# Kernel optimization log

Measured on AMD Instinct MI355X. Metric: run time of the kernel, lower is better.

Reference implementation:

```python
import jax, jax.numpy as jnp
import numpy as np

N_NODES = 100_000
N_EDGES = 6_400_000
THETA = 1.0          # firing threshold
W_SCALE = 0.1        # synaptic weight scale


def setup_inputs() -> dict:
    key = jax.random.key(0)
    k1, k2, k3, k4 = jax.random.split(key, 4)
    src = jax.random.randint(k1, (N_EDGES,), 0, N_NODES)
    dst = jax.random.randint(k2, (N_EDGES,), 0, N_NODES)
    edge_index = jnp.stack([src, dst]).astype(jnp.int64)  # [2, E]
    W = jax.random.normal(k3, (N_EDGES,), dtype=jnp.float32) * W_SCALE
    x = jax.random.uniform(k4, (N_NODES, 1), dtype=jnp.float32)  # initial state window
    return {"x": x, "W": W, "edge_index": edge_index,
            "n_steps": 200, "equilibration_steps": 100}


def _layer(x, src, dst, W):
    # x: [n_nodes, hist]; current spike state is last column (as in x[:, -1])
    s = x[:, -1]
    # synaptic input: scatter-add of weighted presynaptic activity over edges
    inp = jax.ops.segment_sum(W * s[src], dst, num_segments=N_NODES)
    s_new = jax.nn.sigmoid(inp - THETA)  # surrogate spike nonlinearity
    # roll the history window
    return jnp.concatenate([x[:, 1:], s_new[:, None]], axis=1)


def reference(x, W, edge_index, n_steps, equilibration_steps):
    src, dst = edge_index[0], edge_index[1]

    def step(carry, _):
        nxt = _layer(carry, src, dst, W)
        return nxt, nxt[:, -1]

    # equilibration phase (outputs discarded, mirrors _equilibrate)
    x, _ = jax.lax.scan(step, x, None, length=equilibration_steps)
    # recorded simulation phase; dense spike raster replaces the dynamic
    # nonzero()+cat spike log (same information, jit-compatible shape)
    _, raster = jax.lax.scan(step, x, None, length=n_steps)
    return raster  # [n_steps, n_nodes]
```

## Files before the change

### kernel.cpp

```cpp
#include <hip/hip_runtime.h>
#include <math.h>

#define N_NODES 100000
#define N_EDGES 6400000
#define THETA 1.0f
#define EQ_STEPS 100
#define N_STEPS 200
#define TOTAL_STEPS (EQ_STEPS + N_STEPS)

#define NG 1563
#define NRANK (NG * 64)
#define NBINS 512
#define SPLIT 51200
#define C0BYTES 51200
#define C1BYTES 49152
#define S8_BYTES 100352
#define SELL_CAP 10000000
#define WQ_SCALE (32767.0f / 0.75f)
#define QSCALE   (0.75f / (32767.0f * 255.0f))


__global__ __launch_bounds__(256) void deg_kernel(const int* __restrict__ dst,
                                                  int* __restrict__ deg) {
    int stride = gridDim.x * blockDim.x;
    for (int e = blockIdx.x * blockDim.x + threadIdx.x; e < N_EDGES; e += stride)
        atomicAdd(&deg[dst[e]], 1);
}

__global__ __launch_bounds__(256) void binhist_kernel(const int* __restrict__ deg,
                                                      int* __restrict__ bins) {
    int n = blockIdx.x * blockDim.x + threadIdx.x;
    if (n < N_NODES) {
        int d = deg[n]; if (d > NBINS - 1) d = NBINS - 1;
        atomicAdd(&bins[d], 1);
    }
}

__global__ __launch_bounds__(NBINS) void binscan_kernel(const int* __restrict__ bins,
                                                        int* __restrict__ bincur) {
    __shared__ int s[NBINS];
    int t = threadIdx.x;
    s[t] = bins[t];
    __syncthreads();
    for (int o = 1; o < NBINS; o <<= 1) {
        int v = (t >= o) ? s[t - o] : 0;
        __syncthreads();
        s[t] += v;
        __syncthreads();
    }
    bincur[t] = (t == 0) ? 0 : s[t - 1];
}

__global__ __launch_bounds__(256) void perm_kernel(const int* __restrict__ deg,
                                                   int* __restrict__ bincur,
                                                   int* __restrict__ perm,
                                                   int* __restrict__ rank) {
    int n = blockIdx.x * blockDim.x + threadIdx.x;
    if (n < N_NODES) {
        int d = deg[n]; if (d > NBINS - 1) d = NBINS - 1;
        int pos = atomicAdd(&bincur[d], 1);
        perm[pos] = n;
        rank[n] = pos;
    }
}

__global__ __launch_bounds__(256) void degf_kernel(const int* __restrict__ src,
                                                   const int* __restrict__ dst,
                                                   const int* __restrict__ rank,
                                                   int* __restrict__ degf) {
    int stride = gridDim.x * blockDim.x;
    for (int e = blockIdx.x * blockDim.x + threadIdx.x; e < N_EDGES; e += stride) {
        int f = (rank[src[e]] >= SPLIT) ? 1 : 0;
        atomicAdd(&degf[(dst[e] << 1) | f], 1);
    }
}

__global__ __launch_bounds__(256) void width_kernel(const int* __restrict__ degf,
                                                    const int* __restrict__ perm,
                                                    int* __restrict__ gw0,
                                                    int* __restrict__ gw1) {
    int g = blockIdx.x * blockDim.x + threadIdx.x;
    if (g >= NG) return;
    int m0 = 0, m1 = 0;
    for (int j = 0; j < 64; ++j) {
        int r = (g << 6) + j;
        if (r < N_NODES) {
            int n = perm[r];
            int d0 = degf[n << 1], d1 = degf[(n << 1) | 1];
            if (d0 > m0) m0 = d0;
            if (d1 > m1) m1 = d1;
        }
    }
    gw0[g] = (m0 + 3) & ~3;
    gw1[g] = (m1 + 3) & ~3;
}

__global__ __launch_bounds__(1024) void colptr_kernel(const int* __restrict__ gw0,
                                                      const int* __restrict__ gw1,
                                                      int* __restrict__ colptr) {
    __shared__ int sums[1024];
    const int T = 1024;
    int t = threadIdx.x;
    const int PER = (NG + T - 1) / T;
    int b = t * PER;
    int e = b + PER; if (e > NG) e = NG;
    int s = 0;
    for (int i = b; i < e; ++i) s += gw0[i] + gw1[i];
    sums[t] = s;
    __syncthreads();
    for (int o = 1; o < T; o <<= 1) {
        int v = (t >= o) ? sums[t - o] : 0;
        __syncthreads();
        sums[t] += v;
        __syncthreads();
    }
    int base = (t == 0) ? 0 : sums[t - 1];
    for (int i = b; i < e; ++i) {
        colptr[i] = base << 6;
        base += gw0[i] + gw1[i];
    }
    if (t == T - 1) colptr[NG] = base << 6;
}


__global__ __launch_bounds__(256) void sell_scatter_kernel(
        const int* __restrict__ src, const int* __restrict__ dst,
        const float* __restrict__ W,
        const int* __restrict__ rank, const int* __restrict__ colptr,
        const int* __restrict__ gw0,
        int* __restrict__ cnt2, int* __restrict__ sell) {
    int stride = gridDim.x * blockDim.x;
    for (int e = blockIdx.x * blockDim.x + threadIdx.x; e < N_EDGES; e += stride) {
        int d = dst[e];
        int rs = rank[src[e]];
        int f = (rs >= SPLIT) ? 1 : 0;
        int sl = rs - f * SPLIT;
        int k = atomicAdd(&cnt2[(d << 1) | f], 1);
        int rd = rank[d];
        int g = rd >> 6;
        float w = W[e] * WQ_SCALE;
        w = fminf(fmaxf(w, -32767.f), 32767.f);
        int wq = __float2int_rn(w);
        int slot = colptr[g] + ((f ? gw0[g] : 0) << 6)
                 + ((k >> 2) << 8) + ((rd & 63) << 2) + (k & 3);
        sell[slot] = (wq << 16) | sl;
    }
}

__global__ __launch_bounds__(256) void pad_kernel(const int* __restrict__ degf,
                                                  const int* __restrict__ perm,
                                                  const int* __restrict__ colptr,
                                                  const int* __restrict__ gw0,
                                                  int* __restrict__ sell) {
    int r = (blockIdx.x * blockDim.x + threadIdx.x) >> 6;
    int lane = threadIdx.x & 63;
    if (r >= NRANK) return;
    int g = r >> 6;
    int base = colptr[g];
    int w0 = gw0[g];
    int w1 = ((colptr[g + 1] - base) >> 6) - w0;
    int d0 = 0, d1 = 0;
    if (r < N_NODES) {
        int n = perm[r];
        d0 = degf[n << 1]; d1 = degf[(n << 1) | 1];
    }
    int c = (r & 63) << 2;
    for (int k = d0 + lane; k < w0; k += 64)
        sell[base + ((k >> 2) << 8) + c + (k & 3)] = 0;
    int base1 = base + (w0 << 6);
    for (int k = d1 + lane; k < w1; k += 64)
        sell[base1 + ((k >> 2) << 8) + c + (k & 3)] = 0;
}

__global__ __launch_bounds__(256) void initq_kernel(const float* __restrict__ x,
                                                    const int* __restrict__ rank,
                                                    unsigned char* __restrict__ s8) {
    int n = blockIdx.x * blockDim.x + threadIdx.x;
    if (n < N_NODES) {
        float v = fminf(fmaxf(x[n], 0.f), 1.f);
        s8[rank[n]] = (unsigned char)__float2int_rn(v * 255.0f);
    }
}

__global__ __launch_bounds__(1024, 8) void step_kernel(
        const int* __restrict__ sell, const int* __restrict__ colptr,
        const int* __restrict__ gw0, const int* __restrict__ perm,
        const unsigned char* __restrict__ s8_in,
        unsigned char* __restrict__ s8_out,
        float* __restrict__ out_row) {
    __shared__ int4 sc4[C0BYTES / 16];
    __shared__ float red[4][4][64];
    const unsigned char* sc = (const unsigned char*)sc4;
    int tid = threadIdx.x;
    int wv = tid >> 6, lane = tid & 63;
    int gsub = wv >> 2;
    int q = wv & 3;
    int gid = NG - 1 - ((blockIdx.x << 2) + gsub);
    bool active = (gid >= 0);
    int base = 0, wid0 = 0, wid1 = 0;
    if (active) {
        int c0 = colptr[gid], c1 = colptr[gid + 1];
        wid0 = gw0[gid];
        wid1 = ((c1 - c0) >> 6) - wid0;
        base = c0;
    }
    float a0 = 0.f, a1 = 0.f, a2 = 0.f, a3 = 0.f;

    {
        const int4* gp = (const int4*)s8_in;
        for (int i = tid; i < C0BYTES / 16; i += 1024) sc4[i] = gp[i];
    }
    __syncthreads();
    if (active) {
        const int4* col = (const int4*)(sell + base) + lane;
        int n4 = wid0 >> 2;
        #pragma unroll 2
        for (int k = q; k < n4; k += 4) {
            int4 p = col[k << 6];
            a0 = fmaf((float)__mul24(p.x >> 16, (int)sc[p.x & 0xFFFF]), QSCALE, a0);
            a1 = fmaf((float)__mul24(p.y >> 16, (int)sc[p.y & 0xFFFF]), QSCALE, a1);
            a2 = fmaf((float)__mul24(p.z >> 16, (int)sc[p.z & 0xFFFF]), QSCALE, a2);
            a3 = fmaf((float)__mul24(p.w >> 16, (int)sc[p.w & 0xFFFF]), QSCALE, a3);
        }
    }
    __syncthreads();

    {
        const int4* gp = (const int4*)(s8_in + C0BYTES);
        for (int i = tid; i < C1BYTES / 16; i += 1024) sc4[i] = gp[i];
    }
    __syncthreads();
    if (active) {
        const int4* col = (const int4*)(sell + base + (wid0 << 6)) + lane;
        int n4 = wid1 >> 2;
        #pragma unroll 2
        for (int k = q; k < n4; k += 4) {
            int4 p = col[k << 6];
            a0 = fmaf((float)__mul24(p.x >> 16, (int)sc[p.x & 0xFFFF]), QSCALE, a0);
            a1 = fmaf((float)__mul24(p.y >> 16, (int)sc[p.y & 0xFFFF]), QSCALE, a1);
            a2 = fmaf((float)__mul24(p.z >> 16, (int)sc[p.z & 0xFFFF]), QSCALE, a2);
            a3 = fmaf((float)__mul24(p.w >> 16, (int)sc[p.w & 0xFFFF]), QSCALE, a3);
        }
    }
    float acc = (a0 + a1) + (a2 + a3);
    if (q != 0) red[gsub][q][lane] = acc;
    __syncthreads();
    if (q == 0 && active) {
        acc += red[gsub][1][lane] + red[gsub][2][lane] + red[gsub][3][lane];
        int r = (gid << 6) + lane;
        if (r < N_NODES) {
            float v = 1.0f / (1.0f + __expf(-(acc - THETA)));
            s8_out[r] = (unsigned char)__float2int_rn(v * 255.0f);
            if (out_row) out_row[perm[r]] = v;
        }
    }
}

extern "C" void kernel_launch(void* const* d_in, const int* in_sizes, int n_in,
                              void* d_out, int out_size, void* d_ws, size_t ws_size,
                              hipStream_t stream) {
    const float* x  = (const float*)d_in[0];
    const float* W  = (const float*)d_in[1];
    const int*   ei = (const int*)d_in[2];
    const int*   src = ei;
    const int*   dst = ei + N_EDGES;

    char* w = (char*)d_ws;
    size_t o = 0;
    auto alloc = [&](size_t bytes) { char* p = w + o; o = (o + bytes + 511) & ~(size_t)511; return p; };
    int* deg    = (int*)alloc(N_NODES * sizeof(int));
    int* degf   = (int*)alloc((size_t)N_NODES * 2 * sizeof(int));
    int* bins   = (int*)alloc(NBINS * sizeof(int));
    int* bincur = (int*)alloc(NBINS * sizeof(int));
    int* perm   = (int*)alloc(NRANK * sizeof(int));
    int* rank   = (int*)alloc(N_NODES * sizeof(int));
    int* gw0    = (int*)alloc(NG * sizeof(int));
    int* gw1    = (int*)alloc(NG * sizeof(int));
    int* colptr = (int*)alloc((NG + 1) * sizeof(int));
    int* cnt2   = (int*)alloc((size_t)N_NODES * 2 * sizeof(int));
    int* sell   = (int*)alloc((size_t)SELL_CAP * sizeof(int));
    unsigned char* s8a = (unsigned char*)alloc(S8_BYTES);
    unsigned char* s8b = (unsigned char*)alloc(S8_BYTES);

    hipMemsetAsync(deg,  0, N_NODES * sizeof(int), stream);
    hipMemsetAsync(degf, 0, (size_t)N_NODES * 2 * sizeof(int), stream);
    hipMemsetAsync(bins, 0, NBINS * sizeof(int), stream);
    hipMemsetAsync(cnt2, 0, (size_t)N_NODES * 2 * sizeof(int), stream);

    const int NB256 = (N_NODES + 255) / 256;
    deg_kernel<<<1024, 256, 0, stream>>>(dst, deg);
    binhist_kernel<<<NB256, 256, 0, stream>>>(deg, bins);
    binscan_kernel<<<1, NBINS, 0, stream>>>(bins, bincur);
    perm_kernel<<<NB256, 256, 0, stream>>>(deg, bincur, perm, rank);
    degf_kernel<<<1024, 256, 0, stream>>>(src, dst, rank, degf);
    width_kernel<<<(NG + 255) / 256, 256, 0, stream>>>(degf, perm, gw0, gw1);
    colptr_kernel<<<1, 1024, 0, stream>>>(gw0, gw1, colptr);
    sell_scatter_kernel<<<2048, 256, 0, stream>>>(src, dst, W, rank, colptr, gw0, cnt2, sell);
    pad_kernel<<<(NRANK * 64 + 255) / 256, 256, 0, stream>>>(degf, perm, colptr, gw0, sell);
    initq_kernel<<<NB256, 256, 0, stream>>>(x, rank, s8a);

    float* outBase = (float*)d_out;
    unsigned char* bufs[2] = {s8a, s8b};
    const int SGRID = (NG + 3) / 4;
    for (int t = 0; t < TOTAL_STEPS; ++t) {
        unsigned char* cur = bufs[t & 1];
        unsigned char* nxt = bufs[(t + 1) & 1];
        float* outrow = (t >= EQ_STEPS) ? (outBase + (size_t)(t - EQ_STEPS) * N_NODES)
                                        : nullptr;
        step_kernel<<<SGRID, 1024, 0, stream>>>(sell, colptr, gw0, perm, cur, nxt, outrow);
    }
}
```

Baseline: 3.901 ms.

## Balance step-kernel work across blocks and waves by nonzero count

Adds a setup kernel that binary-searches the column pointer so each of 512 blocks gets a contiguous range of row groups holding roughly equal numbers of packed entries. Inside the step kernel, each of the 16 waves takes an even slice of the block's 4-wide work units. Partial sums are combined per group with shared-memory atomics. The aim is to remove load imbalance between blocks and waves. In exchange, each step launches more blocks, so the 100 KB state is staged into shared memory more times in total, and segment tracking plus LDS atomics add overhead. Any block whose range covers more than 16 groups would silently drop the extra groups.

New measurement: 5.587 ms. 1.43x slower.

```diff
diff --git a/kernel.cpp b/kernel.cpp
--- a/kernel.cpp
+++ b/kernel.cpp
@@ -16,6 +16,8 @@
 #define C1BYTES 49152
 #define S8_BYTES 100352
 #define SELL_CAP 10000000
+#define NSB 512
+#define NGPB 16
 #define WQ_SCALE (32767.0f / 0.75f)
 #define QSCALE   (0.75f / (32767.0f * 255.0f))
 
@@ -120,6 +122,20 @@
         base += gw0[i] + gw1[i];
     }
     if (t == T - 1) colptr[NG] = base << 6;
+}
+
+__global__ __launch_bounds__(NSB) void blockmap_kernel(const int* __restrict__ colptr,
+                                                       int* __restrict__ bstart) {
+    long long TS = colptr[NG];
+    int b = threadIdx.x;
+    int lo = 0, hi = NG;
+    while (lo < hi) {
+        int mid = (lo + hi) >> 1;
+        if ((long long)colptr[mid] * NSB < (long long)b * TS) lo = mid + 1;
+        else hi = mid;
+    }
+    bstart[b] = lo;
+    if (b == 0) bstart[NSB] = NG;
 }
 
 
@@ -185,42 +201,70 @@
 __global__ __launch_bounds__(1024, 8) void step_kernel(
         const int* __restrict__ sell, const int* __restrict__ colptr,
         const int* __restrict__ gw0, const int* __restrict__ perm,
+        const int* __restrict__ bstart,
         const unsigned char* __restrict__ s8_in,
         unsigned char* __restrict__ s8_out,
         float* __restrict__ out_row) {
     __shared__ int4 sc4[C0BYTES / 16];
-    __shared__ float red[4][4][64];
+    __shared__ float red[NGPB][64];
+    __shared__ int sb0[NGPB], sb1[NGPB], sn0[NGPB], sn1[NGPB];
+    __shared__ int sq0[NGPB + 1], sq1[NGPB + 1];
     const unsigned char* sc = (const unsigned char*)sc4;
     int tid = threadIdx.x;
     int wv = tid >> 6, lane = tid & 63;
-    int gsub = wv >> 2;
-    int q = wv & 3;
-    int gid = NG - 1 - ((blockIdx.x << 2) + gsub);
-    bool active = (gid >= 0);
-    int base = 0, wid0 = 0, wid1 = 0;
-    if (active) {
-        int c0 = colptr[gid], c1 = colptr[gid + 1];
-        wid0 = gw0[gid];
-        wid1 = ((c1 - c0) >> 6) - wid0;
-        base = c0;
-    }
-    float a0 = 0.f, a1 = 0.f, a2 = 0.f, a3 = 0.f;
+
+    int glo = bstart[blockIdx.x];
+    int ghi = bstart[blockIdx.x + 1];
+    int ng = ghi - glo; if (ng > NGPB) ng = NGPB;
 
     {
         const int4* gp = (const int4*)s8_in;
         for (int i = tid; i < C0BYTES / 16; i += 1024) sc4[i] = gp[i];
     }
-    __syncthreads();
-    if (active) {
-        const int4* col = (const int4*)(sell + base) + lane;
-        int n4 = wid0 >> 2;
-        #pragma unroll 2
-        for (int k = q; k < n4; k += 4) {
-            int4 p = col[k << 6];
-            a0 = fmaf((float)__mul24(p.x >> 16, (int)sc[p.x & 0xFFFF]), QSCALE, a0);
-            a1 = fmaf((float)__mul24(p.y >> 16, (int)sc[p.y & 0xFFFF]), QSCALE, a1);
-            a2 = fmaf((float)__mul24(p.z >> 16, (int)sc[p.z & 0xFFFF]), QSCALE, a2);
-            a3 = fmaf((float)__mul24(p.w >> 16, (int)sc[p.w & 0xFFFF]), QSCALE, a3);
+    if (tid < NGPB * 64) ((float*)red)[tid] = 0.f;
+    if (tid < ng) {
+        int g = glo + tid;
+        int c0 = colptr[g], c1 = colptr[g + 1];
+        int w0 = gw0[g];
+        sb0[tid] = c0;
+        sb1[tid] = c0 + (w0 << 6);
+        sn0[tid] = w0 >> 2;
+        sn1[tid] = (((c1 - c0) >> 6) - w0) >> 2;
+    }
+    __syncthreads();
+    if (tid == 0) {
+        int q0 = 0, q1 = 0;
+        for (int i = 0; i < ng; ++i) {
+            sq0[i] = q0; q0 += sn0[i];
+            sq1[i] = q1; q1 += sn1[i];
+        }
+        sq0[ng] = q0; sq1[ng] = q1;
+    }
+    __syncthreads();
+
+    {
+        int U = sq0[ng];
+        int lo = (wv * U) >> 4, hi = ((wv + 1) * U) >> 4;
+        if (lo < hi) {
+            int seg = 0;
+            while (lo >= sq0[seg + 1]) ++seg;
+            float a0 = 0.f, a1 = 0.f, a2 = 0.f, a3 = 0.f;
+            for (int u = lo; u < hi; ++u) {
+                if (u >= sq0[seg + 1]) {
+                    atomicAdd(&red[seg][lane], (a0 + a1) + (a2 + a3));
+                    a0 = a1 = a2 = a3 = 0.f;
+                    ++seg;
+                    while (u >= sq0[seg + 1]) ++seg;
+                }
+                const int4* cp = (const int4*)(sell + sb0[seg])
+                               + ((u - sq0[seg]) << 6) + lane;
+                int4 pk = *cp;
+                a0 = fmaf((float)__mul24(pk.x >> 16, (int)sc[pk.x & 0xFFFF]), QSCALE, a0);
+                a1 = fmaf((float)__mul24(pk.y >> 16, (int)sc[pk.y & 0xFFFF]), QSCALE, a1);
+                a2 = fmaf((float)__mul24(pk.z >> 16, (int)sc[pk.z & 0xFFFF]), QSCALE, a2);
+                a3 = fmaf((float)__mul24(pk.w >> 16, (int)sc[pk.w & 0xFFFF]), QSCALE, a3);
+            }
+            atomicAdd(&red[seg][lane], (a0 + a1) + (a2 + a3));
         }
     }
     __syncthreads();
@@ -230,26 +274,37 @@
         for (int i = tid; i < C1BYTES / 16; i += 1024) sc4[i] = gp[i];
     }
     __syncthreads();
-    if (active) {
-        const int4* col = (const int4*)(sell + base + (wid0 << 6)) + lane;
-        int n4 = wid1 >> 2;
-        #pragma unroll 2
-        for (int k = q; k < n4; k += 4) {
-            int4 p = col[k << 6];
-            a0 = fmaf((float)__mul24(p.x >> 16, (int)sc[p.x & 0xFFFF]), QSCALE, a0);
-            a1 = fmaf((float)__mul24(p.y >> 16, (int)sc[p.y & 0xFFFF]), QSCALE, a1);
-            a2 = fmaf((float)__mul24(p.z >> 16, (int)sc[p.z & 0xFFFF]), QSCALE, a2);
-            a3 = fmaf((float)__mul24(p.w >> 16, (int)sc[p.w & 0xFFFF]), QSCALE, a3);
-        }
-    }
-    float acc = (a0 + a1) + (a2 + a3);
-    if (q != 0) red[gsub][q][lane] = acc;
-    __syncthreads();
-    if (q == 0 && active) {
-        acc += red[gsub][1][lane] + red[gsub][2][lane] + red[gsub][3][lane];
-        int r = (gid << 6) + lane;
+    {
+        int U = sq1[ng];
+        int lo = (wv * U) >> 4, hi = ((wv + 1) * U) >> 4;
+        if (lo < hi) {
+            int seg = 0;
+            while (lo >= sq1[seg + 1]) ++seg;
+            float a0 = 0.f, a1 = 0.f, a2 = 0.f, a3 = 0.f;
+            for (int u = lo; u < hi; ++u) {
+                if (u >= sq1[seg + 1]) {
+                    atomicAdd(&red[seg][lane], (a0 + a1) + (a2 + a3));
+                    a0 = a1 = a2 = a3 = 0.f;
+                    ++seg;
+                    while (u >= sq1[seg + 1]) ++seg;
+                }
+                const int4* cp = (const int4*)(sell + sb1[seg])
+                               + ((u - sq1[seg]) << 6) + lane;
+                int4 pk = *cp;
+                a0 = fmaf((float)__mul24(pk.x >> 16, (int)sc[pk.x & 0xFFFF]), QSCALE, a0);
+                a1 = fmaf((float)__mul24(pk.y >> 16, (int)sc[pk.y & 0xFFFF]), QSCALE, a1);
+                a2 = fmaf((float)__mul24(pk.z >> 16, (int)sc[pk.z & 0xFFFF]), QSCALE, a2);
+                a3 = fmaf((float)__mul24(pk.w >> 16, (int)sc[pk.w & 0xFFFF]), QSCALE, a3);
+            }
+            atomicAdd(&red[seg][lane], (a0 + a1) + (a2 + a3));
+        }
+    }
+    __syncthreads();
+
+    for (int i = wv; i < ng; i += 16) {
+        int r = ((glo + i) << 6) + lane;
         if (r < N_NODES) {
-            float v = 1.0f / (1.0f + __expf(-(acc - THETA)));
+            float v = 1.0f / (1.0f + __expf(-(red[i][lane] - THETA)));
             s8_out[r] = (unsigned char)__float2int_rn(v * 255.0f);
             if (out_row) out_row[perm[r]] = v;
         }
@@ -277,6 +332,7 @@
     int* gw0    = (int*)alloc(NG * sizeof(int));
     int* gw1    = (int*)alloc(NG * sizeof(int));
     int* colptr = (int*)alloc((NG + 1) * sizeof(int));
+    int* bstart = (int*)alloc((NSB + 1) * sizeof(int));
     int* cnt2   = (int*)alloc((size_t)N_NODES * 2 * sizeof(int));
     int* sell   = (int*)alloc((size_t)SELL_CAP * sizeof(int));
     unsigned char* s8a = (unsigned char*)alloc(S8_BYTES);
@@ -295,18 +351,18 @@
     degf_kernel<<<1024, 256, 0, stream>>>(src, dst, rank, degf);
     width_kernel<<<(NG + 255) / 256, 256, 0, stream>>>(degf, perm, gw0, gw1);
     colptr_kernel<<<1, 1024, 0, stream>>>(gw0, gw1, colptr);
+    blockmap_kernel<<<1, NSB, 0, stream>>>(colptr, bstart);
     sell_scatter_kernel<<<2048, 256, 0, stream>>>(src, dst, W, rank, colptr, gw0, cnt2, sell);
     pad_kernel<<<(NRANK * 64 + 255) / 256, 256, 0, stream>>>(degf, perm, colptr, gw0, sell);
     initq_kernel<<<NB256, 256, 0, stream>>>(x, rank, s8a);
 
     float* outBase = (float*)d_out;
     unsigned char* bufs[2] = {s8a, s8b};
-    const int SGRID = (NG + 3) / 4;
     for (int t = 0; t < TOTAL_STEPS; ++t) {
         unsigned char* cur = bufs[t & 1];
         unsigned char* nxt = bufs[(t + 1) & 1];
         float* outrow = (t >= EQ_STEPS) ? (outBase + (size_t)(t - EQ_STEPS) * N_NODES)
                                         : nullptr;
-        step_kernel<<<SGRID, 1024, 0, stream>>>(sell, colptr, gw0, perm, cur, nxt, outrow);
-    }
-}
+        step_kernel<<<NSB, 1024, 0, stream>>>(sell, colptr, gw0, perm, bstart, cur, nxt, outrow);
+    }
+}
```
